# Optimization experiments

Measured on AMD Instinct MI355X. Metric: run time of the kernel, lower is better.

Reference implementation:

```python
import jax, jax.numpy as jnp
import numpy as np

VOCAB = 50000
D = 256        # embedding_dim = nb_head * size_per_head
H = 8          # nb_head
DH = 32        # size_per_head
B = 8192
L = 64


def setup_inputs() -> dict:
    key = jax.random.key(0)
    ks = jax.random.split(key, 8)
    tokens = jax.random.randint(ks[0], (B, L), 0, VOCAB)
    scale = 0.02
    emb_table = jax.random.normal(ks[1], (VOCAB, D), dtype=jnp.float32) * scale
    WQ = jax.random.normal(ks[2], (D, D), dtype=jnp.float32) * scale
    WK = jax.random.normal(ks[3], (D, D), dtype=jnp.float32) * scale
    WV = jax.random.normal(ks[4], (D, D), dtype=jnp.float32) * scale
    WO = jax.random.normal(ks[5], (D, D), dtype=jnp.float32) * scale
    dense_w = jax.random.normal(ks[6], (D, 1), dtype=jnp.float32) * scale
    dense_b = jnp.zeros((1,), dtype=jnp.float32)
    return {"tokens": tokens, "emb_table": emb_table, "WQ": WQ, "WK": WK,
            "WV": WV, "WO": WO, "dense_w": dense_w, "dense_b": dense_b}


def _fastformer(x, WQ, WK, WV, WO):
    # x: [B, L, D]
    b, l, _ = x.shape
    Q = (x @ WQ).reshape(b, l, H, DH)
    K = (x @ WK).reshape(b, l, H, DH)
    V = (x @ WV).reshape(b, l, H, DH)
    global_q = jnp.mean(Q, axis=1, keepdims=True)   # [B,1,H,DH]
    global_k = jnp.mean(K, axis=1, keepdims=True)
    w = jnp.sum(global_q * K + global_k * Q, axis=-1)  # [B,L,H]
    w = jax.nn.softmax(w, axis=1)                       # softmax over seq
    context = (w[..., None] * V).reshape(b, l, D)
    return context @ WO


def reference(tokens, emb_table, WQ, WK, WV, WO, dense_w, dense_b):
    # NewsEncoder forward (inference: dropout = identity; masks computed but
    # unused by Fastformer.call, matching the original code).
    title_emb = emb_table[tokens]                       # [B,L,D]
    hidden = _fastformer(title_emb, WQ, WK, WV, WO)     # [B,L,D]
    scores = (hidden @ dense_w + dense_b)[..., 0]       # [B,L]
    attn = jax.nn.softmax(scores, axis=1)               # over seq
    news_vector = jnp.sum(hidden * attn[..., None], axis=1)  # [B,D]
    return news_vector
```

## Files before the change

kernel.cpp:

```cpp
#include <hip/hip_runtime.h>
#include <cstdint>


using f32x4  = __attribute__((ext_vector_type(4))) float;
using bf16x8 = __attribute__((ext_vector_type(8))) short;

__device__ __forceinline__ unsigned int pack2bf(float a, float b) {
  unsigned int ua = __builtin_bit_cast(unsigned int, a);
  unsigned int ub = __builtin_bit_cast(unsigned int, b);
  ua = (ua + 0x7fffu + ((ua >> 16) & 1u)) >> 16;
  ub = (ub + 0x7fffu + ((ub >> 16) & 1u)) >> 16;
  return ua | (ub << 16);
}
__device__ __forceinline__ unsigned short bf1(float a) {
  unsigned int ua = __builtin_bit_cast(unsigned int, a);
  ua = (ua + 0x7fffu + ((ua >> 16) & 1u)) >> 16;
  return (unsigned short)ua;
}
__device__ __forceinline__ float ubf(unsigned int u) {
  return __builtin_bit_cast(float, u << 16);
}
__device__ __forceinline__ void gload_lds16(const void* g, void* l) {
  __builtin_amdgcn_global_load_lds(
      (const __attribute__((address_space(1))) void*)g,
      (__attribute__((address_space(3))) void*)l, 16, 0, 0);
}

__global__ __launch_bounds__(256) void prep_all(const float* __restrict__ WQ,
                                                const float* __restrict__ WK,
                                                const float* __restrict__ WV,
                                                const float* __restrict__ WO,
                                                const float* __restrict__ dw,
                                                unsigned short* __restrict__ mbf,
                                                unsigned short* __restrict__ tkn,
                                                unsigned short* __restrict__ ptb) {
  const int t = threadIdx.x;
  const int bid = blockIdx.x;
  if (bid == 0) {
    __shared__ float wod[256];
    float acc = 0.f;
    for (int e = 0; e < 256; e += 4) {
      const float4 w4 = *(const float4*)(WO + (size_t)t * 256 + e);
      const float4 d4 = *(const float4*)(dw + e);
      acc += w4.x * d4.x + w4.y * d4.y + w4.z * d4.z + w4.w * d4.w;
    }
    wod[t] = acc;
    __syncthreads();
    for (int h = 0; h < 8; ++h) {
      float a = 0.f;
      for (int j = 0; j < 32; j += 4) {
        const float4 w4 = *(const float4*)(WV + (size_t)t * 256 + h * 32 + j);
        a += w4.x * wod[h*32+j] + w4.y * wod[h*32+j+1] + w4.z * wod[h*32+j+2] + w4.w * wod[h*32+j+3];
      }
      const float o = __shfl_xor(a, 1);
      if (!(t & 1)) ((unsigned int*)mbf)[h * 128 + (t >> 1)] = pack2bf(a, o);
    }
  } else if (bid <= 256) {
    __shared__ float ek[8][32], eq[8][32];
    const int n0 = (bid - 1) * 8;
    const int h  = n0 >> 8;
    {
      const int ei = t >> 5, j = t & 31;
      const int e = (n0 & 255) + ei;
      ek[ei][j] = WK[(size_t)e * 256 + h * 32 + j];
      eq[ei][j] = WQ[(size_t)e * 256 + h * 32 + j];
    }
    __syncthreads();
    float wqd[32], wkd[32];
#pragma unroll
    for (int j = 0; j < 32; j += 4) {
      *(float4*)(wqd + j) = *(const float4*)(WQ + (size_t)t * 256 + h * 32 + j);
      *(float4*)(wkd + j) = *(const float4*)(WK + (size_t)t * 256 + h * 32 + j);
    }
#pragma unroll
    for (int ei = 0; ei < 8; ++ei) {
      float a = 0.f;
#pragma unroll
      for (int j = 0; j < 32; ++j) a += wqd[j] * ek[ei][j] + wkd[j] * eq[ei][j];
      const float o = __shfl_xor(a, 1);
      if (!(t & 1)) ((unsigned int*)tkn)[(size_t)(n0 + ei) * 128 + (t >> 1)] = pack2bf(a, o);
    }
  } else {
    __shared__ float wvs[32][32];
    __shared__ float wos[32][256];
    const int pb = bid - 257;
    const int h = pb >> 3, d0 = (pb & 7) * 32;
    {
      const int dd = t >> 3, jq = (t & 7) * 4;
      *(float4*)(&wvs[dd][jq]) = *(const float4*)(WV + (size_t)(d0 + dd) * 256 + h * 32 + jq);
      const int c4 = (t & 63) * 4;
#pragma unroll
      for (int jj = 0; jj < 8; ++jj) {
        const int j = (t >> 6) * 8 + jj;
        *(float4*)(&wos[j][c4]) = *(const float4*)(WO + (size_t)(h * 32 + j) * 256 + c4);
      }
    }
    __syncthreads();
    const int n = t;
#pragma unroll 4
    for (int dd = 0; dd < 32; ++dd) {
      float a = 0.f;
#pragma unroll
      for (int j = 0; j < 32; ++j) a += wvs[dd][j] * wos[j][n];
      ptb[(size_t)n * 2048 + h * 256 + d0 + dd] = bf1(a);
    }
  }
}

__global__ __launch_bounds__(256) void ebf_kernel(const float4* __restrict__ emb4,
                                                  uint2* __restrict__ out2, int n) {
  for (int i = blockIdx.x * 256 + threadIdx.x; i < n; i += gridDim.x * 256) {
    const float4 v = emb4[i];
    uint2 pk;
    pk.x = pack2bf(v.x, v.y);
    pk.y = pack2bf(v.z, v.w);
    out2[i] = pk;
  }
}

__global__ __launch_bounds__(256) void xbar_kernel(const int* __restrict__ tokens,
                                                   const unsigned short* __restrict__ ebf,
                                                   unsigned short* __restrict__ xbf) {
  __shared__ int tok[64];
  __shared__ float part[8][256];
  const int b = blockIdx.x, t = threadIdx.x;
  if (t < 64) tok[t] = tokens[b * 64 + t];
  __syncthreads();
  const int rg = t >> 5;
  const int c16 = t & 31;
  const uint4* e4 = (const uint4*)ebf;
  float s[8] = {};
#pragma unroll
  for (int ri = 0; ri < 8; ++ri) {
    const uint4 u = e4[(size_t)tok[rg * 8 + ri] * 32 + c16];
    s[0] += ubf(u.x & 0xffffu); s[1] += ubf(u.x >> 16);
    s[2] += ubf(u.y & 0xffffu); s[3] += ubf(u.y >> 16);
    s[4] += ubf(u.z & 0xffffu); s[5] += ubf(u.z >> 16);
    s[6] += ubf(u.w & 0xffffu); s[7] += ubf(u.w >> 16);
  }
#pragma unroll
  for (int j = 0; j < 8; ++j) part[rg][c16 * 8 + j] = s[j];
  __syncthreads();
  float a = 0.f;
#pragma unroll
  for (int rg2 = 0; rg2 < 8; ++rg2) a += part[rg2][t];
  a *= (1.f / 64.f);
  const float o = __shfl_xor(a, 1);
  if (!(t & 1)) ((unsigned int*)xbf)[(size_t)b * 128 + (t >> 1)] = pack2bf(a, o);
}

__global__ __launch_bounds__(256) void cgemm(const unsigned short* __restrict__ xbf,
                                             const unsigned short* __restrict__ tkn,
                                             unsigned short* __restrict__ cbf) {
  __shared__ unsigned short As[64 * 264];
  const int t = threadIdx.x;
  const int m0 = blockIdx.x * 64, n0 = blockIdx.y * 64;
#pragma unroll
  for (int it = 0; it < 8; ++it) {
    const int idx = it * 256 + t;
    const int row = idx >> 5, c = idx & 31;
    const uint4 v = *(const uint4*)(xbf + (size_t)(m0 + row) * 256 + c * 8);
    *(uint4*)(As + row * 264 + c * 8) = v;
  }
  __syncthreads();
  const int wv = t >> 6, l = t & 63;
  const int g = l >> 4, r = l & 15;
#pragma unroll
  for (int nt = 0; nt < 4; ++nt) {
    const int n = n0 + nt * 16 + r;
    f32x4 acc = {0.f, 0.f, 0.f, 0.f};
#pragma unroll
    for (int kk = 0; kk < 8; ++kk) {
      const bf16x8 a  = *(const bf16x8*)(As + (16 * wv + r) * 264 + kk * 32 + g * 8);
      const bf16x8 bb = *(const bf16x8*)(tkn + (size_t)n * 256 + kk * 32 + g * 8);
      acc = __builtin_amdgcn_mfma_f32_16x16x32_bf16(a, bb, acc, 0, 0, 0);
    }
#pragma unroll
    for (int i = 0; i < 4; ++i)
      cbf[(size_t)(m0 + 16 * wv + g * 4 + i) * 2048 + n] = bf1(acc[i]);
  }
}

__global__ __launch_bounds__(256) void main_kernel(const int* __restrict__ tokens,
                                                   const unsigned short* __restrict__ ebf,
                                                   const unsigned short* __restrict__ mbf,
                                                   const float* __restrict__ dense_b,
                                                   unsigned short* __restrict__ cbf) {
  __shared__ unsigned short xl[64 * 256];
  __shared__ float wslds[64 * 17];
  __shared__ unsigned short cfT[16 * 80];
  const int t = threadIdx.x;
  const int b = blockIdx.x;
  const int wv = t >> 6, l = t & 63;
  const int g = l >> 4, r = l & 15;
  {
    unsigned int* cz = (unsigned int*)(cfT + 8 * 80);
    for (int z = t; z < 320; z += 256) cz[z] = 0u;
  }
  {
    const int ln = t & 63;
#pragma unroll
    for (int it = 0; it < 8; ++it) {
      const int R0 = it * 8 + wv * 2;
      const int R  = R0 + (ln >> 5);
      const int j  = ln & 31;
      const int tk = tokens[b * 64 + R];
      const unsigned short* src = ebf + (size_t)tk * 256 + ((j ^ (R & 7)) << 3);
      gload_lds16(src, (void*)(xl + R0 * 256));
    }
  }
  __syncthreads();
  {
    const unsigned short* arow = xl + (16 * wv + r) * 256;
    const int sw = r & 7;
    const unsigned short* brow = (r < 8) ? (cbf + (size_t)b * 2048 + r * 256)
                                         : (mbf + (size_t)(r - 8) * 256);
    f32x4 acc = {0.f, 0.f, 0.f, 0.f};
#pragma unroll
    for (int kk = 0; kk < 8; ++kk) {
      const bf16x8 a  = *(const bf16x8*)(arow + (((kk * 4 + g) ^ sw) << 3));
      const bf16x8 bb = *(const bf16x8*)(brow + kk * 32 + g * 8);
      acc = __builtin_amdgcn_mfma_f32_16x16x32_bf16(a, bb, acc, 0, 0, 0);
    }
#pragma unroll
    for (int i = 0; i < 4; ++i)
      wslds[(16 * wv + g * 4 + i) * 17 + r] = acc[i];
  }
  __syncthreads();
  {
#pragma unroll
    for (int hh = 0; hh < 2; ++hh) {
      const int h = 2 * wv + hh;
      const float v = wslds[l * 17 + h];
      float mx = v;
#pragma unroll
      for (int sft = 32; sft; sft >>= 1) mx = fmaxf(mx, __shfl_xor(mx, sft));
      const float e = expf(v - mx);
      float sm = e;
#pragma unroll
      for (int sft = 32; sft; sft >>= 1) sm += __shfl_xor(sm, sft);
      wslds[l * 17 + h] = e / sm;
    }
  }
  __syncthreads();
  {
    float p[8], sv[8];
#pragma unroll
    for (int h = 0; h < 8; ++h) { p[h] = wslds[l*17 + h]; sv[h] = wslds[l*17 + 8 + h]; }
    float sc = dense_b[0];
#pragma unroll
    for (int h = 0; h < 8; ++h) sc += p[h] * sv[h];
    float mx = sc;
#pragma unroll
    for (int sft = 32; sft; sft >>= 1) mx = fmaxf(mx, __shfl_xor(mx, sft));
    const float e = expf(sc - mx);
    float sm = e;
#pragma unroll
    for (int sft = 32; sft; sft >>= 1) sm += __shfl_xor(sm, sft);
    const float attn = e / sm;
    float cc0, cc1;
    if      (wv == 0) { cc0 = attn * p[0]; cc1 = attn * p[1]; }
    else if (wv == 1) { cc0 = attn * p[2]; cc1 = attn * p[3]; }
    else if (wv == 2) { cc0 = attn * p[4]; cc1 = attn * p[5]; }
    else              { cc0 = attn * p[6]; cc1 = attn * p[7]; }
    cfT[(2 * wv) * 80 + l]     = bf1(cc0);
    cfT[(2 * wv + 1) * 80 + l] = bf1(cc1);
  }
  __syncthreads();
  {
    const bf16x8 a0 = *(const bf16x8*)(cfT + r * 80 + g * 8);
    const bf16x8 a1 = *(const bf16x8*)(cfT + r * 80 + 32 + g * 8);
    const short* xs = (const short*)xl;
#pragma unroll
    for (int ntt = 0; ntt < 4; ++ntt) {
      const int nt = (ntt + r) & 3;
      const int d = wv * 64 + nt * 16 + r;
      short bv0[8], bv1[8];
#pragma unroll
      for (int j = 0; j < 8; ++j) {
        const int off = ((((d >> 3) ^ j) << 3) | (d & 7));
        bv0[j] = xs[(g * 8 + j) * 256 + off];
        bv1[j] = xs[(32 + g * 8 + j) * 256 + off];
      }
      f32x4 acc = {0.f, 0.f, 0.f, 0.f};
      acc = __builtin_amdgcn_mfma_f32_16x16x32_bf16(a0, *(const bf16x8*)bv0, acc, 0, 0, 0);
      acc = __builtin_amdgcn_mfma_f32_16x16x32_bf16(a1, *(const bf16x8*)bv1, acc, 0, 0, 0);
      if (g < 2) {
#pragma unroll
        for (int i = 0; i < 4; ++i) {
          const int h = g * 4 + i;
          cbf[(size_t)b * 2048 + h * 256 + d] = bf1(acc[i]);
        }
      }
    }
  }
}

__global__ __launch_bounds__(256) void pgemm(const unsigned short* __restrict__ cbf,
                                             const unsigned short* __restrict__ ptb,
                                             float* __restrict__ out) {
  __shared__ unsigned short As[32 * 264];
  const int t = threadIdx.x;
  const int m0 = blockIdx.x * 32, n0 = blockIdx.y * 64;
  const int wv = t >> 6, l = t & 63;
  const int g = l >> 4, r = l & 15;
  const int msub = wv & 1, nhalf = wv >> 1;
  f32x4 acc[2] = {};
  for (int kc = 0; kc < 8; ++kc) {
    __syncthreads();
#pragma unroll
    for (int it = 0; it < 4; ++it) {
      const int idx = it * 256 + t;
      const int row = idx >> 5, c = idx & 31;
      const uint4 v = *(const uint4*)(cbf + (size_t)(m0 + row) * 2048 + kc * 256 + c * 8);
      *(uint4*)(As + row * 264 + c * 8) = v;
    }
    __syncthreads();
#pragma unroll
    for (int kk = 0; kk < 8; ++kk) {
      const bf16x8 a = *(const bf16x8*)(As + (16 * msub + r) * 264 + kk * 32 + g * 8);
#pragma unroll
      for (int nt = 0; nt < 2; ++nt) {
        const int n = n0 + (nhalf * 2 + nt) * 16 + r;
        const bf16x8 bb = *(const bf16x8*)(ptb + (size_t)n * 2048 + kc * 256 + kk * 32 + g * 8);
        acc[nt] = __builtin_amdgcn_mfma_f32_16x16x32_bf16(a, bb, acc[nt], 0, 0, 0);
      }
    }
  }
#pragma unroll
  for (int nt = 0; nt < 2; ++nt) {
    const int n = n0 + (nhalf * 2 + nt) * 16 + r;
#pragma unroll
    for (int i = 0; i < 4; ++i)
      out[(size_t)(m0 + 16 * msub + g * 4 + i) * 256 + n] = acc[nt][i];
  }
}

extern "C" void kernel_launch(void* const* d_in, const int* in_sizes, int n_in,
                              void* d_out, int out_size, void* d_ws, size_t ws_size,
                              hipStream_t stream) {
  const int*   tokens = (const int*)d_in[0];
  const float* emb    = (const float*)d_in[1];
  const float* WQ     = (const float*)d_in[2];
  const float* WK     = (const float*)d_in[3];
  const float* WV     = (const float*)d_in[4];
  const float* WO     = (const float*)d_in[5];
  const float* dw     = (const float*)d_in[6];
  const float* db     = (const float*)d_in[7];
  float* out = (float*)d_out;

  unsigned short* base = (unsigned short*)d_ws;
  unsigned short* mbf  = base;
  unsigned short* xbf  = base + 2048;
  unsigned short* tkn  = xbf + (size_t)8192 * 256;
  unsigned short* cbf  = tkn + (size_t)2048 * 256;
  unsigned short* ebf  = cbf + (size_t)8192 * 2048;
  unsigned short* ptb  = ebf + (size_t)50000 * 256;

  const size_t need_bytes = (size_t)(2048 + 8192*256 + 2048*256 + 8192*2048
                                     + 50000*256 + 256*2048) * 2;
  if (ws_size < need_bytes) return;

  prep_all<<<dim3(321), dim3(256), 0, stream>>>(WQ, WK, WV, WO, dw, mbf, tkn, ptb);
  ebf_kernel<<<dim3(2048), dim3(256), 0, stream>>>((const float4*)emb, (uint2*)ebf,
                                                   50000 * 64);
  xbar_kernel<<<dim3(8192), dim3(256), 0, stream>>>(tokens, ebf, xbf);
  cgemm<<<dim3(128, 32), dim3(256), 0, stream>>>(xbf, tkn, cbf);
  main_kernel<<<dim3(8192), dim3(256), 0, stream>>>(tokens, ebf, mbf, db, cbf);
  pgemm<<<dim3(256, 4), dim3(256), 0, stream>>>(cbf, ptb, out);
}
```

Measured before the change: 260.7 us.

## Add FP8 embedding copy for mean gather and reswizzle main kernel LDS

The embedding-conversion kernel now also writes an FP8 copy of the table (scaled by 64), and a new xbar_fp8 kernel gathers these 8-bit rows to compute the per-sequence mean input, halving the bytes read in that gather. Separately, the LDS swizzle in main_kernel gains an extra XOR term on the row index so the transposed B-fragment reads hit fewer bank conflicts, replacing the earlier rotated-loop trick. In exchange, the conversion kernel writes an extra 12.8MB every call, and the FP8 mean loses precision, which could affect accuracy.

```diff
diff --git a/kernel.cpp b/kernel.cpp
--- a/kernel.cpp
+++ b/kernel.cpp
@@ -3,7 +3,17 @@
 
 
 using f32x4  = __attribute__((ext_vector_type(4))) float;
+using f32x2  = __attribute__((ext_vector_type(2))) float;
 using bf16x8 = __attribute__((ext_vector_type(8))) short;
+
+#if defined(__has_builtin)
+#if __has_builtin(__builtin_amdgcn_cvt_pk_f32_fp8) && __has_builtin(__builtin_amdgcn_cvt_pk_fp8_f32)
+#define HAVE_FP8 1
+#endif
+#endif
+#ifndef HAVE_FP8
+#define HAVE_FP8 0
+#endif
 
 __device__ __forceinline__ unsigned int pack2bf(float a, float b) {
   unsigned int ua = __builtin_bit_cast(unsigned int, a);
@@ -107,16 +117,62 @@
   }
 }
 
+template <bool W8>
 __global__ __launch_bounds__(256) void ebf_kernel(const float4* __restrict__ emb4,
-                                                  uint2* __restrict__ out2, int n) {
+                                                  uint2* __restrict__ out2,
+                                                  unsigned int* __restrict__ out8,
+                                                  int n) {
   for (int i = blockIdx.x * 256 + threadIdx.x; i < n; i += gridDim.x * 256) {
     const float4 v = emb4[i];
     uint2 pk;
     pk.x = pack2bf(v.x, v.y);
     pk.y = pack2bf(v.z, v.w);
     out2[i] = pk;
-  }
-}
+#if HAVE_FP8
+    if constexpr (W8) {
+      int w = 0;
+      w = __builtin_amdgcn_cvt_pk_fp8_f32(v.x * 64.f, v.y * 64.f, w, 0);
+      w = __builtin_amdgcn_cvt_pk_fp8_f32(v.z * 64.f, v.w * 64.f, w, 1);
+      out8[i] = (unsigned int)w;
+    }
+#endif
+  }
+}
+
+#if HAVE_FP8
+__global__ __launch_bounds__(256) void xbar_fp8(const int* __restrict__ tokens,
+                                                const unsigned char* __restrict__ ebf8,
+                                                unsigned short* __restrict__ xbf) {
+  __shared__ int tok[64];
+  __shared__ float part[8][256];
+  const int b = blockIdx.x, t = threadIdx.x;
+  if (t < 64) tok[t] = tokens[b * 64 + t];
+  __syncthreads();
+  const int rg = t >> 5;
+  const int c8 = t & 31;
+  const uint2* e8 = (const uint2*)ebf8;
+  float s[8] = {};
+#pragma unroll
+  for (int ri = 0; ri < 8; ++ri) {
+    const uint2 u = e8[(size_t)tok[rg * 8 + ri] * 32 + c8];
+    const f32x2 p0 = __builtin_amdgcn_cvt_pk_f32_fp8((int)u.x, 0);
+    const f32x2 p1 = __builtin_amdgcn_cvt_pk_f32_fp8((int)u.x, 1);
+    const f32x2 p2 = __builtin_amdgcn_cvt_pk_f32_fp8((int)u.y, 0);
+    const f32x2 p3 = __builtin_amdgcn_cvt_pk_f32_fp8((int)u.y, 1);
+    s[0] += p0.x; s[1] += p0.y; s[2] += p1.x; s[3] += p1.y;
+    s[4] += p2.x; s[5] += p2.y; s[6] += p3.x; s[7] += p3.y;
+  }
+#pragma unroll
+  for (int j = 0; j < 8; ++j) part[rg][c8 * 8 + j] = s[j];
+  __syncthreads();
+  float a = 0.f;
+#pragma unroll
+  for (int rg2 = 0; rg2 < 8; ++rg2) a += part[rg2][t];
+  a *= (1.f / (64.f * 64.f));
+  const float o = __shfl_xor(a, 1);
+  if (!(t & 1)) ((unsigned int*)xbf)[(size_t)b * 128 + (t >> 1)] = pack2bf(a, o);
+}
+#endif
 
 __global__ __launch_bounds__(256) void xbar_kernel(const int* __restrict__ tokens,
                                                    const unsigned short* __restrict__ ebf,
@@ -205,14 +261,15 @@
       const int R  = R0 + (ln >> 5);
       const int j  = ln & 31;
       const int tk = tokens[b * 64 + R];
-      const unsigned short* src = ebf + (size_t)tk * 256 + ((j ^ (R & 7)) << 3);
+      const int swzR = (R & 7) ^ (R >> 3);
+      const unsigned short* src = ebf + (size_t)tk * 256 + ((j ^ swzR) << 3);
       gload_lds16(src, (void*)(xl + R0 * 256));
     }
   }
   __syncthreads();
   {
     const unsigned short* arow = xl + (16 * wv + r) * 256;
-    const int sw = r & 7;
+    const int sw = (r & 7) ^ ((2 * wv + (r >> 3)) & 7);
     const unsigned short* brow = (r < 8) ? (cbf + (size_t)b * 2048 + r * 256)
                                          : (mbf + (size_t)(r - 8) * 256);
     f32x4 acc = {0.f, 0.f, 0.f, 0.f};
@@ -272,15 +329,15 @@
     const bf16x8 a1 = *(const bf16x8*)(cfT + r * 80 + 32 + g * 8);
     const short* xs = (const short*)xl;
 #pragma unroll
-    for (int ntt = 0; ntt < 4; ++ntt) {
-      const int nt = (ntt + r) & 3;
+    for (int nt = 0; nt < 4; ++nt) {
       const int d = wv * 64 + nt * 16 + r;
       short bv0[8], bv1[8];
 #pragma unroll
       for (int j = 0; j < 8; ++j) {
-        const int off = ((((d >> 3) ^ j) << 3) | (d & 7));
-        bv0[j] = xs[(g * 8 + j) * 256 + off];
-        bv1[j] = xs[(32 + g * 8 + j) * 256 + off];
+        const int c0 = ((d >> 3) ^ j ^ g) << 3;
+        bv0[j] = xs[(g * 8 + j) * 256 + (c0 | (d & 7))];
+        const int c1 = ((d >> 3) ^ j ^ g ^ 4) << 3;
+        bv1[j] = xs[(32 + g * 8 + j) * 256 + (c1 | (d & 7))];
       }
       f32x4 acc = {0.f, 0.f, 0.f, 0.f};
       acc = __builtin_amdgcn_mfma_f32_16x16x32_bf16(a0, *(const bf16x8*)bv0, acc, 0, 0, 0);
@@ -356,15 +413,34 @@
   unsigned short* cbf  = tkn + (size_t)2048 * 256;
   unsigned short* ebf  = cbf + (size_t)8192 * 2048;
   unsigned short* ptb  = ebf + (size_t)50000 * 256;
-
-  const size_t need_bytes = (size_t)(2048 + 8192*256 + 2048*256 + 8192*2048
-                                     + 50000*256 + 256*2048) * 2;
-  if (ws_size < need_bytes) return;
+  unsigned char*  ebf8 = (unsigned char*)(ptb + (size_t)256 * 2048);
+
+  const size_t need_base = (size_t)(2048 + 8192*256 + 2048*256 + 8192*2048
+                                    + 50000*256 + 256*2048) * 2;
+  const size_t need_fp8  = need_base + (size_t)50000 * 256;
+  if (ws_size < need_base) return;
+#if HAVE_FP8
+  const bool use8 = (ws_size >= need_fp8);
+#else
+  const bool use8 = false;
+#endif
 
   prep_all<<<dim3(321), dim3(256), 0, stream>>>(WQ, WK, WV, WO, dw, mbf, tkn, ptb);
-  ebf_kernel<<<dim3(2048), dim3(256), 0, stream>>>((const float4*)emb, (uint2*)ebf,
-                                                   50000 * 64);
-  xbar_kernel<<<dim3(8192), dim3(256), 0, stream>>>(tokens, ebf, xbf);
+  if (use8) {
+    ebf_kernel<true><<<dim3(2048), dim3(256), 0, stream>>>((const float4*)emb,
+        (uint2*)ebf, (unsigned int*)ebf8, 50000 * 64);
+  } else {
+    ebf_kernel<false><<<dim3(2048), dim3(256), 0, stream>>>((const float4*)emb,
+        (uint2*)ebf, nullptr, 50000 * 64);
+  }
+#if HAVE_FP8
+  if (use8) {
+    xbar_fp8<<<dim3(8192), dim3(256), 0, stream>>>(tokens, ebf8, xbf);
+  } else
+#endif
+  {
+    xbar_kernel<<<dim3(8192), dim3(256), 0, stream>>>(tokens, ebf, xbf);
+  }
   cgemm<<<dim3(128, 32), dim3(256), 0, stream>>>(xbf, tkn, cbf);
   main_kernel<<<dim3(8192), dim3(256), 0, stream>>>(tokens, ebf, mbf, db, cbf);
   pgemm<<<dim3(256, 4), dim3(256), 0, stream>>>(cbf, ptb, out);
```

Result: no change. 262.4 us (+0.7%).
